# Kernel tuning notes

Measured on AMD Instinct MI355X. Metric: run time of the kernel, lower is better.

The kernel has to match this reference:

```python
import jax, jax.numpy as jnp
import numpy as np

D_MODEL = 1024
NHEAD = 16
D_K = D_MODEL // NHEAD


def setup_inputs() -> dict:
    key = jax.random.key(0)
    ks = jax.random.split(key, 11)
    B, S = 2, 2048
    scale = 1.0 / np.sqrt(D_MODEL)
    inp = {
        "q": jax.random.normal(ks[0], (B, S, D_MODEL), jnp.float32),
        "k": jax.random.normal(ks[1], (B, S, D_MODEL), jnp.float32),
        "v": jax.random.normal(ks[2], (B, S, D_MODEL), jnp.float32),
        "Wq": jax.random.normal(ks[3], (D_MODEL, D_MODEL), jnp.float32) * scale,
        "bq": jnp.zeros((D_MODEL,), jnp.float32),
        "Wk": jax.random.normal(ks[4], (D_MODEL, D_MODEL), jnp.float32) * scale,
        "bk": jnp.zeros((D_MODEL,), jnp.float32),
        "Wv": jax.random.normal(ks[5], (D_MODEL, D_MODEL), jnp.float32) * scale,
        "bv": jnp.zeros((D_MODEL,), jnp.float32),
        "Wo": jax.random.normal(ks[6], (D_MODEL, D_MODEL), jnp.float32) * scale,
        "bo": jnp.zeros((D_MODEL,), jnp.float32),
    }
    return inp


def reference(q, k, v, Wq, bq, Wk, bk, Wv, bv, Wo, bo):
    B, S, _ = q.shape
    # Linear projections (torch Linear: x @ W.T + b), split into heads
    def proj(x, W, b):
        y = jnp.einsum('bsd,ed->bse', x, W) + b
        return y.reshape(B, -1, NHEAD, D_K).transpose(0, 2, 1, 3)  # [B,H,S,Dk]

    qh = proj(q, Wq, bq)
    kh = proj(k, Wk, bk)
    vh = proj(v, Wv, bv)

    scores = jnp.einsum('bhqd,bhkd->bhqk', qh, kh) / jnp.sqrt(
        jnp.asarray(D_K, qh.dtype))
    attn = jax.nn.softmax(scores, axis=-1)  # dropout is identity in eval
    out = jnp.einsum('bhqk,bhkd->bhqd', attn, vh)
    out = out.transpose(0, 2, 1, 3).reshape(B, S, D_MODEL)
    return jnp.einsum('bsd,ed->bse', out, Wo) + bo
```

## Files before the change

### kernel.cpp

```cpp
#include <hip/hip_runtime.h>
#include <stdint.h>
#include <stddef.h>

#define D_MODEL 1024
#define NHEAD   16
#define DK      64
#define BB      2
#define SS      2048
#define NTOK    (BB*SS)

#define SCALE_Q 0.18033688011f

typedef short  short8 __attribute__((ext_vector_type(8)));
typedef __bf16 bf16x8 __attribute__((ext_vector_type(8)));
typedef float  f32x4  __attribute__((ext_vector_type(4)));

__device__ __forceinline__ unsigned short f2bf(float x){
  unsigned int u = __builtin_bit_cast(unsigned int, x);
  u += 0x7fffu + ((u >> 16) & 1u);
  return (unsigned short)(u >> 16);
}

__device__ __forceinline__ unsigned int pack_bf2(float x, float y){
  unsigned int a = __builtin_bit_cast(unsigned int, x) + 0x8000u;
  unsigned int b = __builtin_bit_cast(unsigned int, y) + 0x8000u;
  return __builtin_amdgcn_perm(b, a, 0x07060302u);
}

__device__ __forceinline__ unsigned int cvt_pk_bf16(float lo, float hi){
  unsigned int r;
  asm("v_cvt_pk_bf16_f32 %0, %1, %2" : "=v"(r) : "v"(lo), "v"(hi));
  return r;
}

__device__ __forceinline__ float fast_exp2(float x){
#if __has_builtin(__builtin_amdgcn_exp2f)
  return __builtin_amdgcn_exp2f(x);
#else
  return exp2f(x);
#endif
}

__device__ __forceinline__ f32x4 mfma16(bf16x8 a, bf16x8 b, f32x4 c){
  return __builtin_amdgcn_mfma_f32_16x16x32_bf16(a, b, c, 0, 0, 0);
}

__device__ __forceinline__ void async16(const void* g, void* lds){
  __builtin_amdgcn_global_load_lds(
      (const __attribute__((address_space(1))) unsigned int*)g,
      (__attribute__((address_space(3))) unsigned int*)lds,
      16, 0, 0);
}

__global__ __launch_bounds__(256) void cast_bf16_all(
    const float* __restrict__ q,  const float* __restrict__ k,  const float* __restrict__ v,
    const float* __restrict__ wq, const float* __restrict__ wk, const float* __restrict__ wv,
    const float* __restrict__ wo,
    unsigned short* __restrict__ qb,  unsigned short* __restrict__ kb,  unsigned short* __restrict__ vb,
    unsigned short* __restrict__ wqb, unsigned short* __restrict__ wkb, unsigned short* __restrict__ wvb,
    unsigned short* __restrict__ wob)
{
  const float* src; unsigned short* dst; int n;
  switch (blockIdx.y){
    case 0: src = q;  dst = qb;  n = NTOK*D_MODEL;    break;
    case 1: src = k;  dst = kb;  n = NTOK*D_MODEL;    break;
    case 2: src = v;  dst = vb;  n = NTOK*D_MODEL;    break;
    case 3: src = wq; dst = wqb; n = D_MODEL*D_MODEL; break;
    case 4: src = wk; dst = wkb; n = D_MODEL*D_MODEL; break;
    case 5: src = wv; dst = wvb; n = D_MODEL*D_MODEL; break;
    default: src = wo; dst = wob; n = D_MODEL*D_MODEL; break;
  }
  int i = (blockIdx.x * 256 + threadIdx.x) * 8;
  if (i >= n) return;
  float4 a = *(const float4*)(src + i);
  float4 b = *(const float4*)(src + i + 4);
  short8 o;
  o[0] = (short)f2bf(a.x); o[1] = (short)f2bf(a.y);
  o[2] = (short)f2bf(a.z); o[3] = (short)f2bf(a.w);
  o[4] = (short)f2bf(b.x); o[5] = (short)f2bf(b.y);
  o[6] = (short)f2bf(b.z); o[7] = (short)f2bf(b.w);
  *(short8*)(dst + i) = o;
}

__global__ __launch_bounds__(256) void qkv_gemm(
    const unsigned short* __restrict__ qb, const unsigned short* __restrict__ kb,
    const unsigned short* __restrict__ vb,
    const unsigned short* __restrict__ wqb, const unsigned short* __restrict__ wkb,
    const unsigned short* __restrict__ wvb,
    const float* __restrict__ bq, const float* __restrict__ bk, const float* __restrict__ bv,
    unsigned short* __restrict__ Qh, unsigned short* __restrict__ Kh, unsigned short* __restrict__ Vt)
{
  __shared__ __align__(16) unsigned short S[128*128];
  unsigned short* As0 = S;
  unsigned short* Bs0 = S + 4096;
  unsigned short* As1 = S + 8192;
  unsigned short* Bs1 = S + 12288;

  int bid = blockIdx.x;
  const int id = (bid & 7) * 96 + (bid >> 3);
  const int z = id >> 8, r = id & 255;
  const unsigned short *A, *Bt; const float* bias; unsigned short* C;
  int bm, bn, N, brow; float scale;
  if (z == 0){ A = qb;  Bt = wqb; bias = bq; C = Qh; bm = (r>>3)*128; bn = (r&7)*128; N = 1024; brow = 0; scale = SCALE_Q; }
  else if (z == 1){ A = kb;  Bt = wkb; bias = bk; C = Kh; bm = (r>>3)*128; bn = (r&7)*128; N = 1024; brow = 0; scale = 1.0f; }
  else            { A = wvb; Bt = vb;  bias = bv; C = Vt; bm = (r&7)*128; bn = (r>>3)*128; N = 4096; brow = 1; scale = 1.0f; }
  const int K = 1024;
  const int tid  = threadIdx.x, lane = tid & 63, w = tid >> 6;
  const int quad = lane >> 4,   l16  = lane & 15;
  const int wm = w >> 1, wn = w & 1;
  const int fsl = (quad ^ ((l16 >> 2) & 3)) << 3;

  const unsigned short* asrc[2];
  const unsigned short* bsrc[2];
  #pragma unroll
  for (int c = 0; c < 2; ++c){
    int s = (w*2 + c)*64 + lane;
    int row = s >> 2, c4 = s & 3;
    int cs = (c4 ^ ((row >> 2) & 3)) << 3;
    asrc[c] = A  + (size_t)(bm + row)*K + cs;
    bsrc[c] = Bt + (size_t)(bn + row)*K + cs;
  }

  #pragma unroll
  for (int c = 0; c < 2; ++c){
    async16(asrc[c], (char*)As0 + (w*2 + c)*1024);
    async16(bsrc[c], (char*)Bs0 + (w*2 + c)*1024);
    asrc[c] += 32; bsrc[c] += 32;
  }

  f32x4 acc[4][4] = {};
  for (int t = 0; t < 32; ++t){
    const int cur = t & 1;
    unsigned short* An = cur ? As0 : As1;
    unsigned short* Bn = cur ? Bs0 : Bs1;
    #pragma unroll
    for (int c = 0; c < 2; ++c){
      async16(asrc[c], (char*)An + (w*2 + c)*1024);
      async16(bsrc[c], (char*)Bn + (w*2 + c)*1024);
      asrc[c] += 32; bsrc[c] += 32;
    }
    asm volatile("s_waitcnt vmcnt(4)\n\ts_barrier" ::: "memory");

    const unsigned short* Ac = cur ? As1 : As0;
    const unsigned short* Bc = cur ? Bs1 : Bs0;
    bf16x8 af[4], bf[4];
    #pragma unroll
    for (int mt = 0; mt < 4; ++mt){
      af[mt] = *(const bf16x8*)&Ac[(wm*64 + mt*16 + l16)*32 + fsl];
      bf[mt] = *(const bf16x8*)&Bc[(wn*64 + mt*16 + l16)*32 + fsl];
    }
    #pragma unroll
    for (int mt = 0; mt < 4; ++mt)
      #pragma unroll
      for (int nt = 0; nt < 4; ++nt)
        acc[mt][nt] = mfma16(bf[nt], af[mt], acc[mt][nt]);

    asm volatile("s_waitcnt lgkmcnt(0)\n\ts_barrier" ::: "memory");
  }
  asm volatile("s_waitcnt vmcnt(0)\n\ts_barrier" ::: "memory");

  #pragma unroll
  for (int nt = 0; nt < 4; ++nt){
    int nl = wn*64 + nt*16 + 4*quad;
    float4 b4;
    if (!brow) b4 = *(const float4*)&bias[bn + nl];
    #pragma unroll
    for (int mt = 0; mt < 4; ++mt){
      int ml = wm*64 + mt*16 + l16;
      float bmv = brow ? bias[bm + ml] : 0.0f;
      float v0 = (acc[mt][nt][0] + (brow ? bmv : b4.x)) * scale;
      float v1 = (acc[mt][nt][1] + (brow ? bmv : b4.y)) * scale;
      float v2 = (acc[mt][nt][2] + (brow ? bmv : b4.z)) * scale;
      float v3 = (acc[mt][nt][3] + (brow ? bmv : b4.w)) * scale;
      uint2 p; p.x = pack_bf2(v0, v1); p.y = pack_bf2(v2, v3);
      int gl = nl >> 2;
      if (brow){
        int g3 = gl & 7;
        gl = (gl & ~7) | ((g3 & 3)*2 + (g3 >> 2));
      }
      int gs = gl ^ (ml & 14);
      *(uint2*)&S[ml*128 + gs*4] = p;
    }
  }
  __syncthreads();
  {
    int rr_ = tid >> 1, hf = tid & 1;
    size_t rowbase = (size_t)(bm + rr_) * N + bn;
    #pragma unroll
    for (int i = 0; i < 8; ++i){
      int gg = hf*16 + i*2;
      uint4 d = *(const uint4*)&S[rr_*128 + ((gg ^ (rr_ & 14)) << 2)];
      *(uint4*)&C[rowbase + gg*4] = d;
    }
  }
}

__global__ __launch_bounds__(256) void gemm_out(
    const unsigned short* __restrict__ A, const unsigned short* __restrict__ Bt,
    const float* __restrict__ bias, float* __restrict__ C)
{
  __shared__ __align__(16) unsigned short As[2][64*64];
  __shared__ __align__(16) unsigned short Bs[2][128*64];
  const int K = 1024, N = 1024;
  const int tid  = threadIdx.x, lane = tid & 63, w = tid >> 6;
  const int quad = lane >> 4,   l16  = lane & 15;
  int bid = blockIdx.x;
  const int id = (bid & 7) * 64 + (bid >> 3);
  const int bm = (id >> 3) * 64, bn = (id & 7) * 128;
  const int sw = l16 & 7;

  const unsigned short* asrc[2];
  const unsigned short* bsrc[4];
  #pragma unroll
  for (int c = 0; c < 2; ++c){
    int chunk = (w*2 + c)*64 + lane;
    int row = chunk >> 3, c8 = chunk & 7;
    asrc[c] = A + (size_t)(bm + row)*K + ((c8 ^ (row & 7)) << 3);
  }
  #pragma unroll
  for (int c = 0; c < 4; ++c){
    int chunk = (w*4 + c)*64 + lane;
    int row = chunk >> 3, c8 = chunk & 7;
    bsrc[c] = Bt + (size_t)(bn + row)*K + ((c8 ^ (row & 7)) << 3);
  }

  #pragma unroll
  for (int c = 0; c < 2; ++c){ async16(asrc[c], (char*)As[0] + (w*2 + c)*1024); asrc[c] += 64; }
  #pragma unroll
  for (int c = 0; c < 4; ++c){ async16(bsrc[c], (char*)Bs[0] + (w*4 + c)*1024); bsrc[c] += 64; }

  f32x4 acc[4][2] = {};
  for (int t = 0; t < 16; ++t){
    const int cur = t & 1;
    #pragma unroll
    for (int c = 0; c < 2; ++c){
      async16(asrc[c], (char*)As[1 - cur] + (w*2 + c)*1024); asrc[c] += 64;
    }
    #pragma unroll
    for (int c = 0; c < 4; ++c){
      async16(bsrc[c], (char*)Bs[1 - cur] + (w*4 + c)*1024); bsrc[c] += 64;
    }
    asm volatile("s_waitcnt vmcnt(6)\n\ts_barrier" ::: "memory");

    const unsigned short* Ac = As[cur];
    bf16x8 af[4][2], bf[2][2];
    #pragma unroll
    for (int mt = 0; mt < 4; ++mt)
      #pragma unroll
      for (int ks = 0; ks < 2; ++ks)
        af[mt][ks] = *(const bf16x8*)&Ac[(mt*16 + l16)*64 + (((ks*4 + quad) ^ sw) << 3)];
    #pragma unroll
    for (int nt = 0; nt < 2; ++nt)
      #pragma unroll
      for (int ks = 0; ks < 2; ++ks)
        bf[nt][ks] = *(const bf16x8*)&Bs[cur][(w*32 + nt*16 + l16)*64 + (((ks*4 + quad) ^ sw) << 3)];
    #pragma unroll
    for (int ks = 0; ks < 2; ++ks)
      #pragma unroll
      for (int mt = 0; mt < 4; ++mt)
        #pragma unroll
        for (int nt = 0; nt < 2; ++nt)
          acc[mt][nt] = mfma16(af[mt][ks], bf[nt][ks], acc[mt][nt]);

    asm volatile("s_waitcnt lgkmcnt(0)\n\ts_barrier" ::: "memory");
  }

  #pragma unroll
  for (int mt = 0; mt < 4; ++mt){
    #pragma unroll
    for (int nt = 0; nt < 2; ++nt){
      int col = bn + w*32 + nt*16 + l16;
      float bc = bias[col];
      #pragma unroll
      for (int rr = 0; rr < 4; ++rr){
        int row = bm + mt*16 + quad*4 + rr;
        C[(size_t)row*N + col] = acc[mt][nt][rr] + bc;
      }
    }
  }
}

__global__ __launch_bounds__(512, 4) void attn(
    const unsigned short* __restrict__ Qh, const unsigned short* __restrict__ Kh,
    const unsigned short* __restrict__ Vt, unsigned short* __restrict__ ctx)
{
  __shared__ __align__(16) unsigned short Kbuf[2][64*64];
  __shared__ __align__(16) unsigned short Vbuf[2][64*64];
  __shared__ __align__(16) unsigned short QP[128*64];

  const int tid  = threadIdx.x, lane = tid & 63, w = tid >> 6;
  const int quad = lane >> 4,   l16  = lane & 15;
  const int b = blockIdx.y >> 4, h = blockIdx.y & 15;
  const int q0 = blockIdx.x * 128;
  const int sw = l16 & 7;

  #pragma unroll
  for (int c = 0; c < 2; ++c){
    int s = (w*2 + c)*64 + lane;
    int row = s >> 3, c8 = s & 7;
    async16(Qh + (size_t)(b*SS + q0 + row)*D_MODEL + h*DK + ((c8 ^ (row & 7)) << 3),
            (char*)QP + (w*2 + c)*1024);
  }

  const unsigned short* Kp = Kh + (size_t)(b*SS)*D_MODEL + h*DK;
  const unsigned short* Vp = Vt + (size_t)(h*DK)*NTOK + b*SS;
  const unsigned short* ksrc;
  const unsigned short* vsrc;
  {
    int s = w*64 + lane;
    int row = s >> 3, c8 = s & 7;
    int cs = (c8 ^ (row & 7)) << 3;
    ksrc = Kp + (size_t)row*D_MODEL + cs;
    vsrc = Vp + (size_t)row*NTOK  + cs;
  }

  async16(ksrc, (char*)Kbuf[0] + w*1024);
  async16(vsrc, (char*)Vbuf[0] + w*1024);
  ksrc += 64*D_MODEL;
  vsrc += 64;
  __syncthreads();

  bf16x8 bq[2];
  #pragma unroll
  for (int ks = 0; ks < 2; ++ks)
    bq[ks] = *(const bf16x8*)&QP[(w*16 + l16)*64 + (((ks*4 + quad) ^ sw) << 3)];

  f32x4 acc[4] = {};
  float l0a = 0.0f, l0b = 0.0f;

  for (int it = 0; it < 32; ++it){
    const int cur = it & 1;
    async16(ksrc, (char*)Kbuf[1 - cur] + w*1024);
    async16(vsrc, (char*)Vbuf[1 - cur] + w*1024);
    ksrc += 64*D_MODEL;
    vsrc += 64;
    asm volatile("s_waitcnt vmcnt(2)\n\ts_barrier" ::: "memory");

    const unsigned short* Kc = Kbuf[cur];
    const unsigned short* Vc = Vbuf[cur];

    bf16x8 kf[4][2];
    #pragma unroll
    for (int mt = 0; mt < 4; ++mt)
      #pragma unroll
      for (int ks = 0; ks < 2; ++ks)
        kf[mt][ks] = *(const bf16x8*)&Kc[(mt*16 + l16)*64 + (((ks*4 + quad) ^ sw) << 3)];

    bf16x8 vf[4][2];
    #pragma unroll
    for (int nt = 0; nt < 4; ++nt)
      #pragma unroll
      for (int ks = 0; ks < 2; ++ks)
        vf[nt][ks] = *(const bf16x8*)&Vc[(nt*16 + l16)*64 + (((ks*4 + quad) ^ sw) << 3)];

    f32x4 s0[4] = {};
    #pragma unroll
    for (int mt = 0; mt < 4; ++mt)
      #pragma unroll
      for (int ks = 0; ks < 2; ++ks)
        s0[mt] = mfma16(kf[mt][ks], bq[ks], s0[mt]);

    float sa = 0.0f, sb = 0.0f;
    #pragma unroll
    for (int mt = 0; mt < 4; ++mt)
      #pragma unroll
      for (int rr = 0; rr < 4; ++rr){
        float p0 = fast_exp2(s0[mt][rr]); s0[mt][rr] = p0;
        if (mt & 1) sb += p0; else sa += p0;
      }
    l0a += sa; l0b += sb;

    bf16x8 bp[2];
    #pragma unroll
    for (int ks = 0; ks < 2; ++ks){
      uint4 t;
      t.x = cvt_pk_bf16(s0[2*ks  ][0], s0[2*ks  ][1]);
      t.y = cvt_pk_bf16(s0[2*ks  ][2], s0[2*ks  ][3]);
      t.z = cvt_pk_bf16(s0[2*ks+1][0], s0[2*ks+1][1]);
      t.w = cvt_pk_bf16(s0[2*ks+1][2], s0[2*ks+1][3]);
      bp[ks] = __builtin_bit_cast(bf16x8, t);
    }

    #pragma unroll
    for (int nt = 0; nt < 4; ++nt)
      #pragma unroll
      for (int ks = 0; ks < 2; ++ks)
        acc[nt] = mfma16(vf[nt][ks], bp[ks], acc[nt]);

    asm volatile("s_waitcnt lgkmcnt(0)\n\ts_barrier" ::: "memory");
  }

  float t = l0a + l0b;
  t += __shfl_xor(t, 16);
  t += __shfl_xor(t, 32);
  const float inv = 1.0f / t;

  {
    const int pr = (w*16 + l16)*64;
    #pragma unroll
    for (int nt = 0; nt < 4; ++nt){
      int c8  = nt*2 + (quad >> 1);
      int off = ((c8 ^ sw) << 3) + (quad & 1)*4;
      uint2 p;
      p.x = pack_bf2(acc[nt][0]*inv, acc[nt][1]*inv);
      p.y = pack_bf2(acc[nt][2]*inv, acc[nt][3]*inv);
      *(uint2*)&QP[pr + off] = p;
    }
  }
  asm volatile("s_waitcnt lgkmcnt(0)" ::: "memory");
  {
    int r  = w*16 + (lane >> 2);
    int j0 = lane & 3;
    unsigned short* dst = ctx + (size_t)(b*SS + q0 + r)*D_MODEL + h*DK;
    #pragma unroll
    for (int i = 0; i < 2; ++i){
      int j = j0 + i*4;
      uint4 d = *(const uint4*)&QP[r*64 + ((j ^ (r & 7)) << 3)];
      *(uint4*)(dst + j*8) = d;
    }
  }
}

extern "C" void kernel_launch(void* const* d_in, const int* in_sizes, int n_in,
                              void* d_out, int out_size, void* d_ws, size_t ws_size,
                              hipStream_t stream) {
  const float* q  = (const float*)d_in[0];
  const float* k  = (const float*)d_in[1];
  const float* v  = (const float*)d_in[2];
  const float* Wq = (const float*)d_in[3];
  const float* bq = (const float*)d_in[4];
  const float* Wk = (const float*)d_in[5];
  const float* bk = (const float*)d_in[6];
  const float* Wv = (const float*)d_in[7];
  const float* bv = (const float*)d_in[8];
  const float* Wo = (const float*)d_in[9];
  const float* bo = (const float*)d_in[10];

  char* ws = (char*)d_ws;
  const size_t TOKB = (size_t)NTOK * D_MODEL * 2;
  const size_t WB   = (size_t)D_MODEL * D_MODEL * 2;
  unsigned short* qb  = (unsigned short*)ws;             ws += TOKB;
  unsigned short* kb  = (unsigned short*)ws;             ws += TOKB;
  unsigned short* vb  = (unsigned short*)ws;             ws += TOKB;
  unsigned short* wqb = (unsigned short*)ws;             ws += WB;
  unsigned short* wkb = (unsigned short*)ws;             ws += WB;
  unsigned short* wvb = (unsigned short*)ws;             ws += WB;
  unsigned short* wob = (unsigned short*)ws;             ws += WB;
  unsigned short* Qh  = (unsigned short*)ws;             ws += TOKB;
  unsigned short* Kh  = (unsigned short*)ws;             ws += TOKB;
  unsigned short* Vt  = (unsigned short*)ws;             ws += TOKB;
  unsigned short* ctx = (unsigned short*)ws;             ws += TOKB;
  ws += 4096;

  cast_bf16_all<<<dim3(2048, 7), 256, 0, stream>>>(q, k, v, Wq, Wk, Wv, Wo,
                                                   qb, kb, vb, wqb, wkb, wvb, wob);
  qkv_gemm<<<dim3(768), 256, 0, stream>>>(qb, kb, vb, wqb, wkb, wvb,
                                          bq, bk, bv, Qh, Kh, Vt);
  attn<<<dim3(SS/128, BB*NHEAD), 512, 0, stream>>>(Qh, Kh, Vt, ctx);
  gemm_out<<<dim3(512), 256, 0, stream>>>(ctx, wob, bo, (float*)d_out);
}
```

Baseline: 212.7 us.

## Split attention key tiles across wave pairs with 32-query tiles per wave

Each pair of waves now shares a 32-query tile, and within a pair each wave handles half of every 64-key block. This halves the K-fragment LDS reads per wave and lets each K/V fragment feed two MFMAs, improving register reuse. The two partial PV accumulators and row sums are combined through shared memory at the end. The cost is an extra shared-memory reduction, an added barrier, and more accumulator registers per wave.

```diff
diff --git a/kernel.cpp b/kernel.cpp
--- a/kernel.cpp
+++ b/kernel.cpp
@@ -284,12 +284,15 @@
     const unsigned short* __restrict__ Qh, const unsigned short* __restrict__ Kh,
     const unsigned short* __restrict__ Vt, unsigned short* __restrict__ ctx)
 {
-  __shared__ __align__(16) unsigned short Kbuf[2][64*64];
-  __shared__ __align__(16) unsigned short Vbuf[2][64*64];
-  __shared__ __align__(16) unsigned short QP[128*64];
+  __shared__ __align__(16) unsigned short SH[24576];
+  unsigned short* Kb = SH;
+  unsigned short* Vb = SH + 8192;
+  unsigned short* QP = SH + 16384;
+  __shared__ float lbuf[256];
 
   const int tid  = threadIdx.x, lane = tid & 63, w = tid >> 6;
   const int quad = lane >> 4,   l16  = lane & 15;
+  const int p = w >> 1, hk = w & 1;
   const int b = blockIdx.y >> 4, h = blockIdx.y & 15;
   const int q0 = blockIdx.x * 128;
   const int sw = l16 & 7;
@@ -302,119 +305,149 @@
             (char*)QP + (w*2 + c)*1024);
   }
 
-  const unsigned short* Kp = Kh + (size_t)(b*SS)*D_MODEL + h*DK;
-  const unsigned short* Vp = Vt + (size_t)(h*DK)*NTOK + b*SS;
+  const unsigned short* Kp = Qh;
+  (void)Kp;
   const unsigned short* ksrc;
   const unsigned short* vsrc;
   {
+    const unsigned short* Kpp = Kh + (size_t)(b*SS)*D_MODEL + h*DK;
+    const unsigned short* Vpp = Vt + (size_t)(h*DK)*NTOK + b*SS;
     int s = w*64 + lane;
     int row = s >> 3, c8 = s & 7;
     int cs = (c8 ^ (row & 7)) << 3;
-    ksrc = Kp + (size_t)row*D_MODEL + cs;
-    vsrc = Vp + (size_t)row*NTOK  + cs;
-  }
-
-  async16(ksrc, (char*)Kbuf[0] + w*1024);
-  async16(vsrc, (char*)Vbuf[0] + w*1024);
+    ksrc = Kpp + (size_t)row*D_MODEL + cs;
+    vsrc = Vpp + (size_t)row*NTOK  + cs;
+  }
+
+  async16(ksrc, (char*)Kb + w*1024);
+  async16(vsrc, (char*)Vb + w*1024);
   ksrc += 64*D_MODEL;
   vsrc += 64;
   __syncthreads();
 
-  bf16x8 bq[2];
-  #pragma unroll
-  for (int ks = 0; ks < 2; ++ks)
-    bq[ks] = *(const bf16x8*)&QP[(w*16 + l16)*64 + (((ks*4 + quad) ^ sw) << 3)];
-
-  f32x4 acc[4] = {};
-  float l0a = 0.0f, l0b = 0.0f;
+  bf16x8 bq[2][2];
+  #pragma unroll
+  for (int nq = 0; nq < 2; ++nq)
+    #pragma unroll
+    for (int ks = 0; ks < 2; ++ks)
+      bq[nq][ks] = *(const bf16x8*)&QP[(p*32 + nq*16 + l16)*64 + (((ks*4 + quad) ^ sw) << 3)];
+
+  f32x4 acc[4][2] = {};
+  float l0 = 0.0f, l1 = 0.0f;
 
   for (int it = 0; it < 32; ++it){
     const int cur = it & 1;
-    async16(ksrc, (char*)Kbuf[1 - cur] + w*1024);
-    async16(vsrc, (char*)Vbuf[1 - cur] + w*1024);
+    async16(ksrc, (char*)(Kb + (1 - cur)*4096) + w*1024);
+    async16(vsrc, (char*)(Vb + (1 - cur)*4096) + w*1024);
     ksrc += 64*D_MODEL;
     vsrc += 64;
     asm volatile("s_waitcnt vmcnt(2)\n\ts_barrier" ::: "memory");
 
-    const unsigned short* Kc = Kbuf[cur];
-    const unsigned short* Vc = Vbuf[cur];
-
-    bf16x8 kf[4][2];
-    #pragma unroll
-    for (int mt = 0; mt < 4; ++mt)
+    const unsigned short* Kc = Kb + cur*4096;
+    const unsigned short* Vc = Vb + cur*4096;
+
+    bf16x8 kf[2][2];
+    #pragma unroll
+    for (int mt = 0; mt < 2; ++mt)
       #pragma unroll
       for (int ks = 0; ks < 2; ++ks)
-        kf[mt][ks] = *(const bf16x8*)&Kc[(mt*16 + l16)*64 + (((ks*4 + quad) ^ sw) << 3)];
-
-    bf16x8 vf[4][2];
+        kf[mt][ks] = *(const bf16x8*)&Kc[(hk*32 + mt*16 + l16)*64 + (((ks*4 + quad) ^ sw) << 3)];
+
+    bf16x8 vf[4];
     #pragma unroll
     for (int nt = 0; nt < 4; ++nt)
-      #pragma unroll
-      for (int ks = 0; ks < 2; ++ks)
-        vf[nt][ks] = *(const bf16x8*)&Vc[(nt*16 + l16)*64 + (((ks*4 + quad) ^ sw) << 3)];
-
-    f32x4 s0[4] = {};
-    #pragma unroll
-    for (int mt = 0; mt < 4; ++mt)
-      #pragma unroll
-      for (int ks = 0; ks < 2; ++ks)
-        s0[mt] = mfma16(kf[mt][ks], bq[ks], s0[mt]);
+      vf[nt] = *(const bf16x8*)&Vc[(nt*16 + l16)*64 + (((hk*4 + quad) ^ sw) << 3)];
+
+    f32x4 s0[2][2] = {};
+    #pragma unroll
+    for (int mt = 0; mt < 2; ++mt)
+      #pragma unroll
+      for (int ks = 0; ks < 2; ++ks){
+        s0[mt][0] = mfma16(kf[mt][ks], bq[0][ks], s0[mt][0]);
+        s0[mt][1] = mfma16(kf[mt][ks], bq[1][ks], s0[mt][1]);
+      }
 
     float sa = 0.0f, sb = 0.0f;
     #pragma unroll
-    for (int mt = 0; mt < 4; ++mt)
+    for (int mt = 0; mt < 2; ++mt)
       #pragma unroll
       for (int rr = 0; rr < 4; ++rr){
-        float p0 = fast_exp2(s0[mt][rr]); s0[mt][rr] = p0;
-        if (mt & 1) sb += p0; else sa += p0;
-      }
-    l0a += sa; l0b += sb;
+        float v0 = fast_exp2(s0[mt][0][rr]); s0[mt][0][rr] = v0; sa += v0;
+        float v1 = fast_exp2(s0[mt][1][rr]); s0[mt][1][rr] = v1; sb += v1;
+      }
+    l0 += sa; l1 += sb;
 
     bf16x8 bp[2];
     #pragma unroll
-    for (int ks = 0; ks < 2; ++ks){
+    for (int nq = 0; nq < 2; ++nq){
       uint4 t;
-      t.x = cvt_pk_bf16(s0[2*ks  ][0], s0[2*ks  ][1]);
-      t.y = cvt_pk_bf16(s0[2*ks  ][2], s0[2*ks  ][3]);
-      t.z = cvt_pk_bf16(s0[2*ks+1][0], s0[2*ks+1][1]);
-      t.w = cvt_pk_bf16(s0[2*ks+1][2], s0[2*ks+1][3]);
-      bp[ks] = __builtin_bit_cast(bf16x8, t);
+      t.x = cvt_pk_bf16(s0[0][nq][0], s0[0][nq][1]);
+      t.y = cvt_pk_bf16(s0[0][nq][2], s0[0][nq][3]);
+      t.z = cvt_pk_bf16(s0[1][nq][0], s0[1][nq][1]);
+      t.w = cvt_pk_bf16(s0[1][nq][2], s0[1][nq][3]);
+      bp[nq] = __builtin_bit_cast(bf16x8, t);
     }
 
     #pragma unroll
     for (int nt = 0; nt < 4; ++nt)
       #pragma unroll
-      for (int ks = 0; ks < 2; ++ks)
-        acc[nt] = mfma16(vf[nt][ks], bp[ks], acc[nt]);
+      for (int nq = 0; nq < 2; ++nq)
+        acc[nt][nq] = mfma16(vf[nt], bp[nq], acc[nt][nq]);
 
     asm volatile("s_waitcnt lgkmcnt(0)\n\ts_barrier" ::: "memory");
   }
 
-  float t = l0a + l0b;
-  t += __shfl_xor(t, 16);
-  t += __shfl_xor(t, 32);
-  const float inv = 1.0f / t;
-
-  {
-    const int pr = (w*16 + l16)*64;
-    #pragma unroll
-    for (int nt = 0; nt < 4; ++nt){
-      int c8  = nt*2 + (quad >> 1);
-      int off = ((c8 ^ sw) << 3) + (quad & 1)*4;
-      uint2 p;
-      p.x = pack_bf2(acc[nt][0]*inv, acc[nt][1]*inv);
-      p.y = pack_bf2(acc[nt][2]*inv, acc[nt][3]*inv);
-      *(uint2*)&QP[pr + off] = p;
-    }
-  }
-  asm volatile("s_waitcnt lgkmcnt(0)" ::: "memory");
-  {
-    int r  = w*16 + (lane >> 2);
-    int j0 = lane & 3;
+  asm volatile("s_waitcnt vmcnt(0)\n\ts_barrier" ::: "memory");
+
+  float t0 = l0; t0 += __shfl_xor(t0, 16); t0 += __shfl_xor(t0, 32);
+  float t1 = l1; t1 += __shfl_xor(t1, 16); t1 += __shfl_xor(t1, 32);
+  if (quad == 0){
+    lbuf[(p*2 + hk)*32 +      l16] = t0;
+    lbuf[(p*2 + hk)*32 + 16 + l16] = t1;
+  }
+  float* OS = (float*)SH;
+  if (hk){
+    #pragma unroll
+    for (int nt = 0; nt < 4; ++nt)
+      #pragma unroll
+      for (int nq = 0; nq < 2; ++nq){
+        int qq = nq*16 + l16;
+        int d0 = (nt*16 + quad*4) ^ ((qq & 7) << 2);
+        *(f32x4*)&OS[p*2048 + qq*64 + d0] = acc[nt][nq];
+      }
+  }
+  __syncthreads();
+  if (!hk){
+    float inv0 = 1.0f / (t0 + lbuf[(p*2 + 1)*32 +      l16]);
+    float inv1 = 1.0f / (t1 + lbuf[(p*2 + 1)*32 + 16 + l16]);
+    #pragma unroll
+    for (int nq = 0; nq < 2; ++nq){
+      float inv = nq ? inv1 : inv0;
+      int qq = nq*16 + l16;
+      int pr = (p*32 + qq)*64;
+      #pragma unroll
+      for (int nt = 0; nt < 4; ++nt){
+        int d0 = (nt*16 + quad*4) ^ ((qq & 7) << 2);
+        f32x4 ob = *(const f32x4*)&OS[p*2048 + qq*64 + d0];
+        float v0 = (acc[nt][nq][0] + ob[0]) * inv;
+        float v1 = (acc[nt][nq][1] + ob[1]) * inv;
+        float v2 = (acc[nt][nq][2] + ob[2]) * inv;
+        float v3 = (acc[nt][nq][3] + ob[3]) * inv;
+        int c8  = nt*2 + (quad >> 1);
+        int off = ((c8 ^ sw) << 3) + (quad & 1)*4;
+        uint2 pk;
+        pk.x = pack_bf2(v0, v1);
+        pk.y = pack_bf2(v2, v3);
+        *(uint2*)&QP[pr + off] = pk;
+      }
+    }
+    asm volatile("s_waitcnt lgkmcnt(0)" ::: "memory");
+    int r  = p*32 + (lane >> 1);
+    int j0 = (lane & 1)*4;
     unsigned short* dst = ctx + (size_t)(b*SS + q0 + r)*D_MODEL + h*DK;
     #pragma unroll
-    for (int i = 0; i < 2; ++i){
-      int j = j0 + i*4;
+    for (int i = 0; i < 4; ++i){
+      int j = j0 + i;
       uint4 d = *(const uint4*)&QP[r*64 + ((j ^ (r & 7)) << 3)];
       *(uint4*)(dst + j*8) = d;
     }
```

Result: no change. 211.7 us (-0.5%).
